# Performance work log

Measured on AMD Instinct MI355X. Metric: run time of the kernel, lower is better.

The kernel has to match this reference:

```python
import jax, jax.numpy as jnp
import numpy as np

B, S, E, H = 4, 2048, 512, 8
D = E // H  # head dim
CDIM = 3


def setup_inputs() -> dict:
    key = jax.random.key(0)
    ks = jax.random.split(key, 16)
    inp = {
        'q': jax.random.normal(ks[0], (B, S, E), jnp.float32),
        'k': jax.random.normal(ks[1], (B, S, E), jnp.float32),
        'v': jax.random.normal(ks[2], (B, S, E), jnp.float32),
        'coords_q': jax.random.normal(ks[3], (B, S, CDIM), jnp.float32),
        'coords_k': jax.random.normal(ks[4], (B, S, CDIM), jnp.float32),
        'attn_mask': jax.random.randint(ks[5], (B, S, S), 0, 2).astype(bool),
        'alibi_mask': jax.random.randint(ks[6], (B, S, S), 0, 2).astype(bool),
        # per-head projection params, stacked over heads: [H, E, D]
        'Wq': jax.random.normal(ks[7], (H, E, D), jnp.float32) / np.sqrt(E),
        'bq': jnp.zeros((H, D), jnp.float32),
        'Wk': jax.random.normal(ks[8], (H, E, D), jnp.float32) / np.sqrt(E),
        'bk': jnp.zeros((H, D), jnp.float32),
        'Wv': jax.random.normal(ks[9], (H, E, D), jnp.float32) / np.sqrt(E),
        'bv': jnp.zeros((H, D), jnp.float32),
        # per-head ALiBi params; running_mean is a buffer (eval mode -> constant ones)
        'bias_scale': jax.random.uniform(ks[10], (H,), jnp.float32),
        'running_mean': jnp.ones((H,), jnp.float32),
        # output projection
        'fc_w': jax.random.normal(ks[11], (E, E), jnp.float32) / np.sqrt(E),
        'fc_b': jnp.zeros((E,), jnp.float32),
    }
    return inp


def reference(q, k, v, coords_q, coords_k, attn_mask, alibi_mask,
              Wq, bq, Wk, bk, Wv, bv, bias_scale, running_mean, fc_w, fc_b):
    # per-head projections, vectorized over heads: [B,H,S,D]
    qh = jnp.einsum('bse,hed->bhsd', q, Wq) + bq[None, :, None, :]
    kh = jnp.einsum('bse,hed->bhsd', k, Wk) + bk[None, :, None, :]
    vh = jnp.einsum('bse,hed->bhsd', v, Wv) + bv[None, :, None, :]

    # scaled dot-product logits: [B,H,Sq,Sk]
    logits = jnp.einsum('bhqd,bhkd->bhqk', qh, kh) * (D ** -0.5)
    weights = jax.nn.softmax(logits, axis=-1)

    # pairwise euclidean distances between coords: [B,Sq,Sk]
    diff = coords_q[:, :, None, :] - coords_k[:, None, :, :]
    dist = jnp.sqrt(jnp.sum(diff * diff, axis=-1))

    # per-head distance bias (eval: divide by running_mean buffer, scale by bias_scale)
    scale = (bias_scale / running_mean)[None, :, None, None]  # [1,H,1,1]
    scaled_dist = dist[:, None, :, :] * scale                  # [B,H,Sq,Sk]
    masked_dist = jnp.where(~alibi_mask[:, None, :, :], scaled_dist, 0.0)

    # post-softmax bias subtraction and masking (non-standard attention)
    masked = jnp.where(~attn_mask[:, None, :, :], weights - masked_dist, 0.0)

    att = jnp.einsum('bhqk,bhkd->bhqd', masked, vh)            # [B,H,S,D]
    att = att.transpose(0, 2, 1, 3).reshape(B, S, E)           # [B,S,E]
    return att @ fc_w.T + fc_b
```

## Files before the change

kernel.cpp:

```cpp
#include <hip/hip_runtime.h>

typedef unsigned short ushort;
typedef unsigned char uchar;
typedef unsigned long long u64;
typedef __attribute__((ext_vector_type(8))) short short8;
typedef __attribute__((ext_vector_type(4))) float f32x4;
typedef __attribute__((ext_vector_type(4))) unsigned int uint4v;

#define B_ 4
#define S_ 2048
#define E_ 512
#define H_ 8
#define D_ 64
#define LDT 40
#define LDF 68

__device__ inline ushort f2bf(float f) {
  union { float f; unsigned int u; } v; v.f = f;
  unsigned int u = v.u;
  unsigned int r = u + 0x7FFFu + ((u >> 16) & 1u);
  return (ushort)(r >> 16);
}

__device__ inline unsigned int cvt_pk_bf16(float a, float b) {
  unsigned int r;
  asm("v_cvt_pk_bf16_f32 %0, %1, %2" : "=v"(r) : "v"(a), "v"(b));
  return r;
}

__device__ inline float exp2_fast(float x) {
#if defined(__has_builtin)
#if __has_builtin(__builtin_amdgcn_exp2f)
  return __builtin_amdgcn_exp2f(x);
#else
  return __expf(x * 0.69314718056f);
#endif
#else
  return __expf(x * 0.69314718056f);
#endif
}

__device__ inline short8 mask_keep(short8 p, short8 a2) {
  union U { short8 s; uint4v u; } P, A;
  P.s = p; A.s = a2;
#pragma unroll
  for (int i = 0; i < 4; ++i) {
    unsigned int t = A.u[i] & 0x80008000u;
    unsigned int dm = (t >> 15) * 0xFFFFu;
    P.u[i] &= ~dm;
  }
  return P.s;
}

__device__ inline float dpp_sum16(float v) {
  union { float f; int i; } s, t;
  s.f = v;
  t.i = __builtin_amdgcn_update_dpp(0, s.i, 0x128, 0xf, 0xf, false); s.f += t.f;
  t.i = __builtin_amdgcn_update_dpp(0, s.i, 0x124, 0xf, 0xf, false); s.f += t.f;
  t.i = __builtin_amdgcn_update_dpp(0, s.i, 0x122, 0xf, 0xf, false); s.f += t.f;
  t.i = __builtin_amdgcn_update_dpp(0, s.i, 0x121, 0xf, 0xf, false); s.f += t.f;
  return s.f;
}

__global__ void detect_kernel(const uchar* __restrict__ am, int* flag) {
  __shared__ int s;
  if (threadIdx.x == 0) s = 0;
  __syncthreads();
  int x = 0;
  for (int p = threadIdx.x; p < 4096; p += 256)
    if (p & 3) x += am[p];
  atomicAdd(&s, x);
  __syncthreads();
  if (threadIdx.x == 0) *flag = (s == 0) ? 1 : 0;
}

__global__ __launch_bounds__(256) void convert_w_kernel(
    const float* __restrict__ Wq, const float* __restrict__ Wk, const float* __restrict__ Wv,
    ushort* __restrict__ wt) {
  const int p = blockIdx.y;
  const float* W = (p == 0) ? Wq : (p == 1) ? Wk : Wv;
  const int n = blockIdx.x;
  const int h = n >> 6, d = n & 63;
  ushort* o = wt + ((size_t)p * E_ + n) * E_;
  for (int e = threadIdx.x; e < E_; e += 256)
    o[e] = f2bf(W[((size_t)h * E_ + e) * D_ + d]);
}

__global__ __launch_bounds__(256) void convert_fcw_kernel(
    const float* __restrict__ fcw, ushort* __restrict__ fcwbf) {
  size_t base = ((size_t)blockIdx.x * 256 + threadIdx.x) * 8;
  float4 a = *(const float4*)&fcw[base];
  float4 b = *(const float4*)&fcw[base + 4];
  short8 o;
  o[0] = (short)f2bf(a.x); o[1] = (short)f2bf(a.y); o[2] = (short)f2bf(a.z); o[3] = (short)f2bf(a.w);
  o[4] = (short)f2bf(b.x); o[5] = (short)f2bf(b.y); o[6] = (short)f2bf(b.z); o[7] = (short)f2bf(b.w);
  *(short8*)&fcwbf[base] = o;
}

__global__ __launch_bounds__(256) void proj_gemm_kernel(
    const float* __restrict__ qx, const float* __restrict__ kx, const float* __restrict__ vx,
    const ushort* __restrict__ wt,
    const float* __restrict__ bq, const float* __restrict__ bk, const float* __restrict__ bv,
    ushort* __restrict__ qkv) {
  const int phys = blockIdx.x;
  const int logical = (phys & 7) * 96 + (phys >> 3);
  const int p = logical >> 8;
  const int rem = logical & 255;
  const int m0 = (rem >> 2) * 128, n0 = (rem & 3) * 128;

  const float* A   = (p == 0) ? qx : (p == 1) ? kx : vx;
  const ushort* Bt = wt + (size_t)p * (E_ * E_);
  const float* bias = (p == 0) ? bq : (p == 1) ? bk : bv;
  const float osc = (p == 0) ? 0.125f * 1.44269504f : 1.0f;
  ushort* out = qkv + (size_t)p * (B_ * H_ * S_ * D_);

  const int tid = threadIdx.x;
  const int w = tid >> 6, lane = tid & 63;
  const int g = lane >> 4, c = lane & 15;
  const int wr = w >> 1, wc = w & 1;

  __shared__ ushort As[128][LDT], Bs[128][LDT];

  f32x4 acc[4][4];
#pragma unroll
  for (int i = 0; i < 4; ++i)
#pragma unroll
    for (int j = 0; j < 4; ++j) acc[i][j] = (f32x4){0, 0, 0, 0};

  const int srow = tid >> 2, sc8 = (tid & 3) * 8;
  float4 pa0[2], pa1[2];
  short8 pb[2];
#pragma unroll
  for (int it = 0; it < 2; ++it) {
    const float* ap = &A[(size_t)(m0 + srow + 64 * it) * E_ + sc8];
    pa0[it] = *(const float4*)ap;
    pa1[it] = *(const float4*)(ap + 4);
    pb[it] = *(const short8*)&Bt[(size_t)(n0 + srow + 64 * it) * E_ + sc8];
  }

  for (int kk = 0; kk < E_; kk += 32) {
    __syncthreads();
#pragma unroll
    for (int it = 0; it < 2; ++it) {
      unsigned int r0 = cvt_pk_bf16(pa0[it].x, pa0[it].y), r1 = cvt_pk_bf16(pa0[it].z, pa0[it].w);
      unsigned int r2 = cvt_pk_bf16(pa1[it].x, pa1[it].y), r3 = cvt_pk_bf16(pa1[it].z, pa1[it].w);
      short8 av;
      av[0] = (short)(ushort)r0; av[1] = (short)(ushort)(r0 >> 16);
      av[2] = (short)(ushort)r1; av[3] = (short)(ushort)(r1 >> 16);
      av[4] = (short)(ushort)r2; av[5] = (short)(ushort)(r2 >> 16);
      av[6] = (short)(ushort)r3; av[7] = (short)(ushort)(r3 >> 16);
      *(short8*)&As[srow + 64 * it][sc8] = av;
      *(short8*)&Bs[srow + 64 * it][sc8] = pb[it];
    }
    __syncthreads();
    if (kk + 32 < E_) {
#pragma unroll
      for (int it = 0; it < 2; ++it) {
        const float* ap = &A[(size_t)(m0 + srow + 64 * it) * E_ + kk + 32 + sc8];
        pa0[it] = *(const float4*)ap;
        pa1[it] = *(const float4*)(ap + 4);
        pb[it] = *(const short8*)&Bt[(size_t)(n0 + srow + 64 * it) * E_ + kk + 32 + sc8];
      }
    }
    short8 af[4], bfr[4];
#pragma unroll
    for (int i = 0; i < 4; ++i) af[i] = *(const short8*)&As[wr * 64 + i * 16 + c][8 * g];
#pragma unroll
    for (int j = 0; j < 4; ++j) bfr[j] = *(const short8*)&Bs[wc * 64 + j * 16 + c][8 * g];
#pragma unroll
    for (int i = 0; i < 4; ++i)
#pragma unroll
      for (int j = 0; j < 4; ++j)
        acc[i][j] = __builtin_amdgcn_mfma_f32_16x16x32_bf16(af[i], bfr[j], acc[i][j], 0, 0, 0);
  }

#pragma unroll
  for (int i = 0; i < 4; ++i)
#pragma unroll
    for (int jj = 0; jj < 4; ++jj) {
      int grow = m0 + wr * 64 + i * 16 + 4 * g + jj;
      int b = grow >> 11, s = grow & 2047;
#pragma unroll
      for (int j = 0; j < 4; ++j) {
        int col = n0 + wc * 64 + j * 16 + c;
        int h = col >> 6, d = col & 63;
        out[(((size_t)(b * H_ + h)) * S_ + s) * D_ + d] = f2bf((acc[i][j][jj] + bias[col]) * osc);
      }
    }
}

__global__ __launch_bounds__(256) void transpose_v_kernel(
    const ushort* __restrict__ vh, ushort* __restrict__ vtg) {
  const int bh = blockIdx.y, s0 = blockIdx.x * 64;
  __shared__ ushort tile[64][70];
  const int tid = threadIdx.x;
#pragma unroll
  for (int it = 0; it < 2; ++it) {
    int chunk = tid + 256 * it;
    int r = chunk >> 3, c8 = chunk & 7;
    *(short8*)&tile[r][c8 * 8] = *(const short8*)&vh[((size_t)bh * S_ + s0 + r) * D_ + c8 * 8];
  }
  __syncthreads();
#pragma unroll
  for (int it = 0; it < 2; ++it) {
    int chunk = tid + 256 * it;
    int d = chunk >> 3, s8 = chunk & 7;
    short8 o;
#pragma unroll
    for (int j = 0; j < 8; ++j) o[j] = (short)tile[s8 * 8 + j][d];
    *(short8*)&vtg[((size_t)bh * D_ + d) * S_ + s0 + s8 * 8] = o;
  }
}

__global__ __launch_bounds__(256) void m2dist_kernel(
    const float* __restrict__ cq, const float* __restrict__ ck,
    const void* __restrict__ am_raw, const void* __restrict__ alm_raw,
    const int* __restrict__ flag,
    ushort* __restrict__ m2d) {
  const bool isInt = (*flag != 0);
  const int b = blockIdx.y, qi = blockIdx.x;
  const int k0 = threadIdx.x * 8;
  const size_t rowbase = ((size_t)b * S_ + qi) * S_;
  const float qx = cq[((size_t)b * S_ + qi) * 3 + 0];
  const float qy = cq[((size_t)b * S_ + qi) * 3 + 1];
  const float qz = cq[((size_t)b * S_ + qi) * 3 + 2];
  int a[8], al[8];
  if (isInt) {
    int4 A0 = *(const int4*)&((const int*)am_raw)[rowbase + k0];
    int4 A1 = *(const int4*)&((const int*)am_raw)[rowbase + k0 + 4];
    int4 L0 = *(const int4*)&((const int*)alm_raw)[rowbase + k0];
    int4 L1 = *(const int4*)&((const int*)alm_raw)[rowbase + k0 + 4];
    a[0]=A0.x; a[1]=A0.y; a[2]=A0.z; a[3]=A0.w; a[4]=A1.x; a[5]=A1.y; a[6]=A1.z; a[7]=A1.w;
    al[0]=L0.x; al[1]=L0.y; al[2]=L0.z; al[3]=L0.w; al[4]=L1.x; al[5]=L1.y; al[6]=L1.z; al[7]=L1.w;
  } else {
    u64 ab = *(const u64*)&((const uchar*)am_raw)[rowbase + k0];
    u64 lb = *(const u64*)&((const uchar*)alm_raw)[rowbase + k0];
#pragma unroll
    for (int j = 0; j < 8; ++j) { a[j] = (int)((ab >> (8 * j)) & 0xFF); al[j] = (int)((lb >> (8 * j)) & 0xFF); }
  }
  float c24[24];
  {
    const float* ckp = ck + ((size_t)b * S_ + k0) * 3;
#pragma unroll
    for (int t = 0; t < 6; ++t) {
      float4 cv = *(const float4*)(ckp + 4 * t);
      c24[4 * t] = cv.x; c24[4 * t + 1] = cv.y; c24[4 * t + 2] = cv.z; c24[4 * t + 3] = cv.w;
    }
  }
  float dist[8];
#pragma unroll
  for (int j = 0; j < 8; ++j) {
    const float dx = qx - c24[3 * j], dy = qy - c24[3 * j + 1], dz = qz - c24[3 * j + 2];
    dist[j] = sqrtf(dx * dx + dy * dy + dz * dz);
  }
  short8 md;
#pragma unroll
  for (int jp = 0; jp < 4; ++jp) {
    unsigned int r = cvt_pk_bf16(dist[2 * jp], dist[2 * jp + 1]);
    ushort v0 = (!a[2 * jp]     && !al[2 * jp])     ? (ushort)r         : (ushort)0;
    ushort v1 = (!a[2 * jp + 1] && !al[2 * jp + 1]) ? (ushort)(r >> 16) : (ushort)0;
    if (a[2 * jp])     v0 |= 0x8000u;
    if (a[2 * jp + 1]) v1 |= 0x8000u;
    md[2 * jp] = (short)v0; md[2 * jp + 1] = (short)v1;
  }
  *(short8*)&m2d[rowbase + k0] = md;
}

__global__ __launch_bounds__(256) void flash_kernel(
    const ushort* __restrict__ qh, const ushort* __restrict__ kh, const ushort* __restrict__ vtg,
    const ushort* __restrict__ m2d,
    const float* __restrict__ bscale, const float* __restrict__ rmean,
    ushort* __restrict__ attb) {
  const int flat = blockIdx.x;
  const int h = flat >> 6;
  const int grp = flat & 63;
  const int b = grp >> 4;
  const int qb = (grp & 15) * 128;
  const int bh = b * 8 + h;
  const int tid = threadIdx.x;
  const int w = tid >> 6, lane = tid & 63;
  const int g = lane >> 4, c = lane & 15;

  __shared__ ushort Kt[2][64][LDF];
  __shared__ ushort Vt[2][64][LDF];
  __shared__ ushort Pl[4][32][LDF];

  const size_t bhS = (size_t)bh * S_;
  const int qr0 = qb + 16 * w + c;
  const int qr1 = qr0 + 64;
  const short8 aq0 = *(const short8*)(qh + (bhS + qr0) * D_ + 8 * g);
  const short8 aq1 = *(const short8*)(qh + (bhS + qr0) * D_ + 8 * g + 32);
  const short8 aq2 = *(const short8*)(qh + (bhS + qr1) * D_ + 8 * g);
  const short8 aq3 = *(const short8*)(qh + (bhS + qr1) * D_ + 8 * g + 32);

  const int skr = tid >> 3, sc8 = (tid & 7) * 8;
  const ushort* pk0 = kh + (bhS + skr) * D_ + sc8;
  const ushort* pk1 = pk0 + 32 * D_;
  const ushort* pv0 = vtg + ((size_t)bh * D_ + skr) * S_ + sc8;
  const ushort* pv1 = pv0 + 32 * S_;
  const ushort* pm0 = m2d + ((size_t)b * S_ + qr0) * S_ + 8 * g;
  const ushort* pm1 = pm0 + 32;
  const ushort* pm2 = m2d + ((size_t)b * S_ + qr1) * S_ + 8 * g;
  const ushort* pm3 = pm2 + 32;

  f32x4 acc1g0[4], acc2g0[4], acc1g1[4], acc2g1[4];
#pragma unroll
  for (int t = 0; t < 4; ++t) {
    acc1g0[t] = (f32x4){0,0,0,0}; acc2g0[t] = (f32x4){0,0,0,0};
    acc1g1[t] = (f32x4){0,0,0,0}; acc2g1[t] = (f32x4){0,0,0,0};
  }
  float l0[4] = {0, 0, 0, 0}, l1[4] = {0, 0, 0, 0};

  *(short8*)&Kt[0][skr][sc8]      = *(const short8*)pk0;  pk0 += 64 * D_;
  *(short8*)&Kt[0][skr + 32][sc8] = *(const short8*)pk1;  pk1 += 64 * D_;
  *(short8*)&Vt[0][skr][sc8]      = *(const short8*)pv0;  pv0 += 64;
  *(short8*)&Vt[0][skr + 32][sc8] = *(const short8*)pv1;  pv1 += 64;
  short8 a2n0 = *(const short8*)pm0; pm0 += 64;
  short8 a2n1 = *(const short8*)pm1; pm1 += 64;
  short8 a2n2 = *(const short8*)pm2; pm2 += 64;
  short8 a2n3 = *(const short8*)pm3; pm3 += 64;
  short8 skn0 = *(const short8*)pk0;  pk0 += 64 * D_;
  short8 skn1 = *(const short8*)pk1;  pk1 += 64 * D_;
  short8 svn0 = *(const short8*)pv0;  pv0 += 64;
  short8 svn1 = *(const short8*)pv1;  pv1 += 64;
  __syncthreads();

  for (int kb = 0; kb < S_; kb += 64) {
    const int cur = (kb >> 6) & 1;
    short8 a2c0 = a2n0, a2c1 = a2n1, a2c2 = a2n2, a2c3 = a2n3;
    a2n0 = *(const short8*)pm0; pm0 += 64;
    a2n1 = *(const short8*)pm1; pm1 += 64;
    a2n2 = *(const short8*)pm2; pm2 += 64;
    a2n3 = *(const short8*)pm3; pm3 += 64;

    f32x4 sf0[4], sf1[4];
    __builtin_amdgcn_s_setprio(1);
#pragma unroll
    for (int t = 0; t < 4; ++t) {
      short8 b0 = *(const short8*)&Kt[cur][16 * t + c][8 * g];
      short8 b1 = *(const short8*)&Kt[cur][16 * t + c][8 * g + 32];
      f32x4 z0 = (f32x4){0, 0, 0, 0}, z1 = (f32x4){0, 0, 0, 0};
      z0 = __builtin_amdgcn_mfma_f32_16x16x32_bf16(aq0, b0, z0, 0, 0, 0);
      z0 = __builtin_amdgcn_mfma_f32_16x16x32_bf16(aq1, b1, z0, 0, 0, 0);
      z1 = __builtin_amdgcn_mfma_f32_16x16x32_bf16(aq2, b0, z1, 0, 0, 0);
      z1 = __builtin_amdgcn_mfma_f32_16x16x32_bf16(aq3, b1, z1, 0, 0, 0);
      sf0[t] = z0; sf1[t] = z1;
    }
    __builtin_amdgcn_s_setprio(0);

#pragma unroll
    for (int t = 0; t < 4; ++t)
#pragma unroll
      for (int jp = 0; jp < 2; ++jp) {
        float p0 = exp2_fast(sf0[t][2 * jp]);
        float p1 = exp2_fast(sf0[t][2 * jp + 1]);
        l0[2 * jp] += p0; l0[2 * jp + 1] += p1;
        unsigned int r = cvt_pk_bf16(p0, p1);
        Pl[w][4 * g + 2 * jp][16 * t + c]     = (ushort)r;
        Pl[w][4 * g + 2 * jp + 1][16 * t + c] = (ushort)(r >> 16);
        float p2 = exp2_fast(sf1[t][2 * jp]);
        float p3 = exp2_fast(sf1[t][2 * jp + 1]);
        l1[2 * jp] += p2; l1[2 * jp + 1] += p3;
        unsigned int r2 = cvt_pk_bf16(p2, p3);
        Pl[w][16 + 4 * g + 2 * jp][16 * t + c]     = (ushort)r2;
        Pl[w][16 + 4 * g + 2 * jp + 1][16 * t + c] = (ushort)(r2 >> 16);
      }

    asm volatile("s_waitcnt lgkmcnt(0)" ::: "memory");
    __builtin_amdgcn_sched_barrier(0);

    short8 pa0 = *(const short8*)&Pl[w][c][8 * g];
    short8 pa1 = *(const short8*)&Pl[w][c][8 * g + 32];
    short8 pa2 = *(const short8*)&Pl[w][16 + c][8 * g];
    short8 pa3 = *(const short8*)&Pl[w][16 + c][8 * g + 32];
    pa0 = mask_keep(pa0, a2c0);
    pa1 = mask_keep(pa1, a2c1);
    pa2 = mask_keep(pa2, a2c2);
    pa3 = mask_keep(pa3, a2c3);
    __builtin_amdgcn_s_setprio(1);
#pragma unroll
    for (int t2 = 0; t2 < 4; ++t2) {
      short8 v0 = *(const short8*)&Vt[cur][16 * t2 + c][8 * g];
      short8 v1 = *(const short8*)&Vt[cur][16 * t2 + c][8 * g + 32];
      acc1g0[t2] = __builtin_amdgcn_mfma_f32_16x16x32_bf16(pa0, v0, acc1g0[t2], 0, 0, 0);
      acc1g0[t2] = __builtin_amdgcn_mfma_f32_16x16x32_bf16(pa1, v1, acc1g0[t2], 0, 0, 0);
      acc2g0[t2] = __builtin_amdgcn_mfma_f32_16x16x32_bf16(a2c0, v0, acc2g0[t2], 0, 0, 0);
      acc2g0[t2] = __builtin_amdgcn_mfma_f32_16x16x32_bf16(a2c1, v1, acc2g0[t2], 0, 0, 0);
      acc1g1[t2] = __builtin_amdgcn_mfma_f32_16x16x32_bf16(pa2, v0, acc1g1[t2], 0, 0, 0);
      acc1g1[t2] = __builtin_amdgcn_mfma_f32_16x16x32_bf16(pa3, v1, acc1g1[t2], 0, 0, 0);
      acc2g1[t2] = __builtin_amdgcn_mfma_f32_16x16x32_bf16(a2c2, v0, acc2g1[t2], 0, 0, 0);
      acc2g1[t2] = __builtin_amdgcn_mfma_f32_16x16x32_bf16(a2c3, v1, acc2g1[t2], 0, 0, 0);
    }
    __builtin_amdgcn_s_setprio(0);

    if (kb + 64 < S_) {
      *(short8*)&Kt[cur ^ 1][skr][sc8]      = skn0;
      *(short8*)&Kt[cur ^ 1][skr + 32][sc8] = skn1;
      *(short8*)&Vt[cur ^ 1][skr][sc8]      = svn0;
      *(short8*)&Vt[cur ^ 1][skr + 32][sc8] = svn1;
      skn0 = *(const short8*)pk0;  pk0 += 64 * D_;
      skn1 = *(const short8*)pk1;  pk1 += 64 * D_;
      svn0 = *(const short8*)pv0;  pv0 += 64;
      svn1 = *(const short8*)pv1;  pv1 += 64;
    }
    __syncthreads();
  }

  float linv0[4], linv1[4];
#pragma unroll
  for (int j = 0; j < 4; ++j) {
    linv0[j] = 1.0f / dpp_sum16(l0[j]);
    linv1[j] = 1.0f / dpp_sum16(l1[j]);
  }
  const float scale = bscale[h] / rmean[h];
#pragma unroll
  for (int t2 = 0; t2 < 4; ++t2)
#pragma unroll
    for (int j = 0; j < 4; ++j) {
      int qrA = qb + 16 * w + 4 * g + j;
      int d = 16 * t2 + c;
      attb[(((size_t)b * S_ + qrA) * H_ + h) * D_ + d] =
          f2bf(acc1g0[t2][j] * linv0[j] - scale * acc2g0[t2][j]);
      attb[(((size_t)b * S_ + qrA + 64) * H_ + h) * D_ + d] =
          f2bf(acc1g1[t2][j] * linv1[j] - scale * acc2g1[t2][j]);
    }
}

__global__ __launch_bounds__(256) void final_gemm_kernel(
    const ushort* __restrict__ attb, const ushort* __restrict__ fcwbf,
    const float* __restrict__ fcb, float* __restrict__ out) {
  const int phys = blockIdx.x;
  const int logical = (phys & 7) * 32 + (phys >> 3);
  const int m0 = (logical >> 2) * 128, n0 = (logical & 3) * 128;
  const int tid = threadIdx.x;
  const int w = tid >> 6, lane = tid & 63;
  const int g = lane >> 4, c = lane & 15;
  const int wr = w >> 1, wc = w & 1;

  __shared__ ushort As[128][LDT], Bs[128][LDT];

  f32x4 acc[4][4];
#pragma unroll
  for (int i = 0; i < 4; ++i)
#pragma unroll
    for (int j = 0; j < 4; ++j) acc[i][j] = (f32x4){0, 0, 0, 0};

  const int srow = tid >> 2, sc8 = (tid & 3) * 8;
  short8 pa[2], pb[2];
#pragma unroll
  for (int it = 0; it < 2; ++it) {
    pa[it] = *(const short8*)&attb[(size_t)(m0 + srow + 64 * it) * E_ + sc8];
    pb[it] = *(const short8*)&fcwbf[(size_t)(n0 + srow + 64 * it) * E_ + sc8];
  }

  for (int kk = 0; kk < E_; kk += 32) {
    __syncthreads();
#pragma unroll
    for (int it = 0; it < 2; ++it) {
      *(short8*)&As[srow + 64 * it][sc8] = pa[it];
      *(short8*)&Bs[srow + 64 * it][sc8] = pb[it];
    }
    __syncthreads();
    if (kk + 32 < E_) {
#pragma unroll
      for (int it = 0; it < 2; ++it) {
        pa[it] = *(const short8*)&attb[(size_t)(m0 + srow + 64 * it) * E_ + kk + 32 + sc8];
        pb[it] = *(const short8*)&fcwbf[(size_t)(n0 + srow + 64 * it) * E_ + kk + 32 + sc8];
      }
    }
    short8 af[4], bfr[4];
#pragma unroll
    for (int i = 0; i < 4; ++i) af[i] = *(const short8*)&As[wr * 64 + i * 16 + c][8 * g];
#pragma unroll
    for (int j = 0; j < 4; ++j) bfr[j] = *(const short8*)&Bs[wc * 64 + j * 16 + c][8 * g];
#pragma unroll
    for (int i = 0; i < 4; ++i)
#pragma unroll
      for (int j = 0; j < 4; ++j)
        acc[i][j] = __builtin_amdgcn_mfma_f32_16x16x32_bf16(af[i], bfr[j], acc[i][j], 0, 0, 0);
  }

#pragma unroll
  for (int i = 0; i < 4; ++i)
#pragma unroll
    for (int jj = 0; jj < 4; ++jj) {
      int grow = m0 + wr * 64 + i * 16 + 4 * g + jj;
#pragma unroll
      for (int j = 0; j < 4; ++j) {
        int col = n0 + wc * 64 + j * 16 + c;
        out[(size_t)grow * E_ + col] = acc[i][j][jj] + fcb[col];
      }
    }
}

extern "C" void kernel_launch(void* const* d_in, const int* in_sizes, int n_in,
                              void* d_out, int out_size, void* d_ws, size_t ws_size,
                              hipStream_t stream) {
  const float* q   = (const float*)d_in[0];
  const float* k   = (const float*)d_in[1];
  const float* v   = (const float*)d_in[2];
  const float* cq  = (const float*)d_in[3];
  const float* ck  = (const float*)d_in[4];
  const void*  am  = d_in[5];
  const void*  alm = d_in[6];
  const float* Wq  = (const float*)d_in[7];
  const float* bq  = (const float*)d_in[8];
  const float* Wk  = (const float*)d_in[9];
  const float* bk  = (const float*)d_in[10];
  const float* Wv  = (const float*)d_in[11];
  const float* bv  = (const float*)d_in[12];
  const float* bsc = (const float*)d_in[13];
  const float* rm  = (const float*)d_in[14];
  const float* fcw = (const float*)d_in[15];
  const float* fcb = (const float*)d_in[16];
  float* out = (float*)d_out;

  char* ws = (char*)d_ws;
  ushort* attb = (ushort*)(ws);
  ushort* vtg  = (ushort*)(ws + 16ull * 1024 * 1024);
  ushort* qkv  = (ushort*)(ws + 24ull * 1024 * 1024);
  ushort* m2d  = (ushort*)(ws + 48ull * 1024 * 1024);
  ushort* wt   = (ushort*)(ws + 80ull * 1024 * 1024);
  ushort* fcwbf= (ushort*)(ws + 80ull * 1024 * 1024 + 1536 * 1024);
  int*    flag = (int*)   (ws + 82ull * 1024 * 1024);

  ushort* qh = qkv;
  ushort* kh = qkv + (size_t)(B_ * H_ * S_ * D_);
  ushort* vh = qkv + 2 * (size_t)(B_ * H_ * S_ * D_);

  detect_kernel<<<1, 256, 0, stream>>>((const uchar*)am, flag);
  convert_w_kernel<<<dim3(512, 3), 256, 0, stream>>>(Wq, Wk, Wv, wt);
  convert_fcw_kernel<<<128, 256, 0, stream>>>(fcw, fcwbf);
  proj_gemm_kernel<<<768, 256, 0, stream>>>(q, k, v, wt, bq, bk, bv, qkv);
  transpose_v_kernel<<<dim3(S_ / 64, B_ * H_), 256, 0, stream>>>(vh, vtg);
  m2dist_kernel<<<dim3(S_, B_), 256, 0, stream>>>(cq, ck, am, alm, flag, m2d);
  flash_kernel<<<512, 256, 0, stream>>>(qh, kh, vtg, m2d, bsc, rm, attb);
  final_gemm_kernel<<<256, 256, 0, stream>>>(attb, fcwbf, fcb, out);
}
```

Baseline: 176.6 us.

## Split key range across two wave groups in flash kernel with LDS reduction

Doubles the flash attention block to 512 threads: two groups of four waves each handle alternating 64-key tiles for the same query rows, then combine their accumulators and row sums through shared memory. The probability tile buffer is halved and the two query sub-tiles are processed one after another. K/V staging moves from LDS double buffering to register prefetch with two barriers per iteration. This aims to raise wave-level parallelism and latency hiding, at the cost of extra syncs, a final reduction, and more serialized exp/MFMA phases.

```diff
diff --git a/kernel.cpp b/kernel.cpp
--- a/kernel.cpp
+++ b/kernel.cpp
@@ -266,7 +266,7 @@
   *(short8*)&m2d[rowbase + k0] = md;
 }
 
-__global__ __launch_bounds__(256) void flash_kernel(
+__global__ __launch_bounds__(512) void flash_kernel(
     const ushort* __restrict__ qh, const ushort* __restrict__ kh, const ushort* __restrict__ vtg,
     const ushort* __restrict__ m2d,
     const float* __restrict__ bscale, const float* __restrict__ rmean,
@@ -280,13 +280,14 @@
   const int tid = threadIdx.x;
   const int w = tid >> 6, lane = tid & 63;
   const int g = lane >> 4, c = lane & 15;
-
-  __shared__ ushort Kt[2][64][LDF];
-  __shared__ ushort Vt[2][64][LDF];
-  __shared__ ushort Pl[4][32][LDF];
+  const int wq = w & 3, wh = w >> 2;
+
+  __shared__ __align__(16) ushort Kt[2][64][LDF];
+  __shared__ __align__(16) ushort Vt[2][64][LDF];
+  __shared__ __align__(16) ushort Pl[8][16][LDF];
 
   const size_t bhS = (size_t)bh * S_;
-  const int qr0 = qb + 16 * w + c;
+  const int qr0 = qb + 16 * wq + c;
   const int qr1 = qr0 + 64;
   const short8 aq0 = *(const short8*)(qh + (bhS + qr0) * D_ + 8 * g);
   const short8 aq1 = *(const short8*)(qh + (bhS + qr0) * D_ + 8 * g + 32);
@@ -295,12 +296,12 @@
 
   const int skr = tid >> 3, sc8 = (tid & 7) * 8;
   const ushort* pk0 = kh + (bhS + skr) * D_ + sc8;
-  const ushort* pk1 = pk0 + 32 * D_;
+  const ushort* pk1 = pk0 + 64 * D_;
   const ushort* pv0 = vtg + ((size_t)bh * D_ + skr) * S_ + sc8;
-  const ushort* pv1 = pv0 + 32 * S_;
-  const ushort* pm0 = m2d + ((size_t)b * S_ + qr0) * S_ + 8 * g;
+  const ushort* pv1 = pv0 + 64;
+  const ushort* pm0 = m2d + ((size_t)b * S_ + qr0) * S_ + wh * 64 + 8 * g;
   const ushort* pm1 = pm0 + 32;
-  const ushort* pm2 = m2d + ((size_t)b * S_ + qr1) * S_ + 8 * g;
+  const ushort* pm2 = m2d + ((size_t)b * S_ + qr1) * S_ + wh * 64 + 8 * g;
   const ushort* pm3 = pm2 + 32;
 
   f32x4 acc1g0[4], acc2g0[4], acc1g1[4], acc2g1[4];
@@ -311,34 +312,39 @@
   }
   float l0[4] = {0, 0, 0, 0}, l1[4] = {0, 0, 0, 0};
 
-  *(short8*)&Kt[0][skr][sc8]      = *(const short8*)pk0;  pk0 += 64 * D_;
-  *(short8*)&Kt[0][skr + 32][sc8] = *(const short8*)pk1;  pk1 += 64 * D_;
-  *(short8*)&Vt[0][skr][sc8]      = *(const short8*)pv0;  pv0 += 64;
-  *(short8*)&Vt[0][skr + 32][sc8] = *(const short8*)pv1;  pv1 += 64;
-  short8 a2n0 = *(const short8*)pm0; pm0 += 64;
-  short8 a2n1 = *(const short8*)pm1; pm1 += 64;
-  short8 a2n2 = *(const short8*)pm2; pm2 += 64;
-  short8 a2n3 = *(const short8*)pm3; pm3 += 64;
-  short8 skn0 = *(const short8*)pk0;  pk0 += 64 * D_;
-  short8 skn1 = *(const short8*)pk1;  pk1 += 64 * D_;
-  short8 svn0 = *(const short8*)pv0;  pv0 += 64;
-  short8 svn1 = *(const short8*)pv1;  pv1 += 64;
-  __syncthreads();
-
-  for (int kb = 0; kb < S_; kb += 64) {
-    const int cur = (kb >> 6) & 1;
+  short8 sk0 = *(const short8*)pk0;  pk0 += 128 * D_;
+  short8 sk1 = *(const short8*)pk1;  pk1 += 128 * D_;
+  short8 sv0 = *(const short8*)pv0;  pv0 += 128;
+  short8 sv1 = *(const short8*)pv1;  pv1 += 128;
+  short8 a2n0 = *(const short8*)pm0; pm0 += 128;
+  short8 a2n1 = *(const short8*)pm1; pm1 += 128;
+  short8 a2n2 = *(const short8*)pm2; pm2 += 128;
+  short8 a2n3 = *(const short8*)pm3; pm3 += 128;
+
+  for (int i = 0; i < 16; ++i) {
+    __syncthreads();
+    *(short8*)&Kt[0][skr][sc8] = sk0;
+    *(short8*)&Kt[1][skr][sc8] = sk1;
+    *(short8*)&Vt[0][skr][sc8] = sv0;
+    *(short8*)&Vt[1][skr][sc8] = sv1;
+    __syncthreads();
+
     short8 a2c0 = a2n0, a2c1 = a2n1, a2c2 = a2n2, a2c3 = a2n3;
-    a2n0 = *(const short8*)pm0; pm0 += 64;
-    a2n1 = *(const short8*)pm1; pm1 += 64;
-    a2n2 = *(const short8*)pm2; pm2 += 64;
-    a2n3 = *(const short8*)pm3; pm3 += 64;
+    sk0 = *(const short8*)pk0;  pk0 += 128 * D_;
+    sk1 = *(const short8*)pk1;  pk1 += 128 * D_;
+    sv0 = *(const short8*)pv0;  pv0 += 128;
+    sv1 = *(const short8*)pv1;  pv1 += 128;
+    a2n0 = *(const short8*)pm0; pm0 += 128;
+    a2n1 = *(const short8*)pm1; pm1 += 128;
+    a2n2 = *(const short8*)pm2; pm2 += 128;
+    a2n3 = *(const short8*)pm3; pm3 += 128;
 
     f32x4 sf0[4], sf1[4];
     __builtin_amdgcn_s_setprio(1);
 #pragma unroll
     for (int t = 0; t < 4; ++t) {
-      short8 b0 = *(const short8*)&Kt[cur][16 * t + c][8 * g];
-      short8 b1 = *(const short8*)&Kt[cur][16 * t + c][8 * g + 32];
+      short8 b0 = *(const short8*)&Kt[wh][16 * t + c][8 * g];
+      short8 b1 = *(const short8*)&Kt[wh][16 * t + c][8 * g + 32];
       f32x4 z0 = (f32x4){0, 0, 0, 0}, z1 = (f32x4){0, 0, 0, 0};
       z0 = __builtin_amdgcn_mfma_f32_16x16x32_bf16(aq0, b0, z0, 0, 0, 0);
       z0 = __builtin_amdgcn_mfma_f32_16x16x32_bf16(aq1, b1, z0, 0, 0, 0);
@@ -358,30 +364,39 @@
         unsigned int r = cvt_pk_bf16(p0, p1);
         Pl[w][4 * g + 2 * jp][16 * t + c]     = (ushort)r;
         Pl[w][4 * g + 2 * jp + 1][16 * t + c] = (ushort)(r >> 16);
-        float p2 = exp2_fast(sf1[t][2 * jp]);
-        float p3 = exp2_fast(sf1[t][2 * jp + 1]);
-        l1[2 * jp] += p2; l1[2 * jp + 1] += p3;
-        unsigned int r2 = cvt_pk_bf16(p2, p3);
-        Pl[w][16 + 4 * g + 2 * jp][16 * t + c]     = (ushort)r2;
-        Pl[w][16 + 4 * g + 2 * jp + 1][16 * t + c] = (ushort)(r2 >> 16);
-      }
-
+      }
     asm volatile("s_waitcnt lgkmcnt(0)" ::: "memory");
     __builtin_amdgcn_sched_barrier(0);
-
     short8 pa0 = *(const short8*)&Pl[w][c][8 * g];
     short8 pa1 = *(const short8*)&Pl[w][c][8 * g + 32];
-    short8 pa2 = *(const short8*)&Pl[w][16 + c][8 * g];
-    short8 pa3 = *(const short8*)&Pl[w][16 + c][8 * g + 32];
     pa0 = mask_keep(pa0, a2c0);
     pa1 = mask_keep(pa1, a2c1);
+    asm volatile("s_waitcnt lgkmcnt(0)" ::: "memory");
+    __builtin_amdgcn_sched_barrier(0);
+
+#pragma unroll
+    for (int t = 0; t < 4; ++t)
+#pragma unroll
+      for (int jp = 0; jp < 2; ++jp) {
+        float p0 = exp2_fast(sf1[t][2 * jp]);
+        float p1 = exp2_fast(sf1[t][2 * jp + 1]);
+        l1[2 * jp] += p0; l1[2 * jp + 1] += p1;
+        unsigned int r = cvt_pk_bf16(p0, p1);
+        Pl[w][4 * g + 2 * jp][16 * t + c]     = (ushort)r;
+        Pl[w][4 * g + 2 * jp + 1][16 * t + c] = (ushort)(r >> 16);
+      }
+    asm volatile("s_waitcnt lgkmcnt(0)" ::: "memory");
+    __builtin_amdgcn_sched_barrier(0);
+    short8 pa2 = *(const short8*)&Pl[w][c][8 * g];
+    short8 pa3 = *(const short8*)&Pl[w][c][8 * g + 32];
     pa2 = mask_keep(pa2, a2c2);
     pa3 = mask_keep(pa3, a2c3);
+
     __builtin_amdgcn_s_setprio(1);
 #pragma unroll
     for (int t2 = 0; t2 < 4; ++t2) {
-      short8 v0 = *(const short8*)&Vt[cur][16 * t2 + c][8 * g];
-      short8 v1 = *(const short8*)&Vt[cur][16 * t2 + c][8 * g + 32];
+      short8 v0 = *(const short8*)&Vt[wh][16 * t2 + c][8 * g];
+      short8 v1 = *(const short8*)&Vt[wh][16 * t2 + c][8 * g + 32];
       acc1g0[t2] = __builtin_amdgcn_mfma_f32_16x16x32_bf16(pa0, v0, acc1g0[t2], 0, 0, 0);
       acc1g0[t2] = __builtin_amdgcn_mfma_f32_16x16x32_bf16(pa1, v1, acc1g0[t2], 0, 0, 0);
       acc2g0[t2] = __builtin_amdgcn_mfma_f32_16x16x32_bf16(a2c0, v0, acc2g0[t2], 0, 0, 0);
@@ -392,38 +407,67 @@
       acc2g1[t2] = __builtin_amdgcn_mfma_f32_16x16x32_bf16(a2c3, v1, acc2g1[t2], 0, 0, 0);
     }
     __builtin_amdgcn_s_setprio(0);
-
-    if (kb + 64 < S_) {
-      *(short8*)&Kt[cur ^ 1][skr][sc8]      = skn0;
-      *(short8*)&Kt[cur ^ 1][skr + 32][sc8] = skn1;
-      *(short8*)&Vt[cur ^ 1][skr][sc8]      = svn0;
-      *(short8*)&Vt[cur ^ 1][skr + 32][sc8] = svn1;
-      skn0 = *(const short8*)pk0;  pk0 += 64 * D_;
-      skn1 = *(const short8*)pk1;  pk1 += 64 * D_;
-      svn0 = *(const short8*)pv0;  pv0 += 64;
-      svn1 = *(const short8*)pv1;  pv1 += 64;
-    }
-    __syncthreads();
-  }
-
-  float linv0[4], linv1[4];
-#pragma unroll
-  for (int j = 0; j < 4; ++j) {
-    linv0[j] = 1.0f / dpp_sum16(l0[j]);
-    linv1[j] = 1.0f / dpp_sum16(l1[j]);
-  }
-  const float scale = bscale[h] / rmean[h];
-#pragma unroll
-  for (int t2 = 0; t2 < 4; ++t2)
+  }
+
+  float* cA = (float*)&Kt[0][0][0];
+  float* cB = (float*)&Vt[0][0][0];
+  float* cC = (float*)&Pl[0][0][0];
+  const int cidx = (wq * 64 + lane) * 16;
+  __syncthreads();
+  if (wh == 1) {
+#pragma unroll
+    for (int t = 0; t < 4; ++t) {
+      *(f32x4*)&cA[cidx + 4 * t] = acc1g0[t];
+      *(f32x4*)&cB[cidx + 4 * t] = acc1g1[t];
+      *(f32x4*)&cC[cidx + 4 * t] = acc2g0[t];
+    }
+  }
+  __syncthreads();
+  if (wh == 0) {
+#pragma unroll
+    for (int t = 0; t < 4; ++t) {
+      acc1g0[t] += *(const f32x4*)&cA[cidx + 4 * t];
+      acc1g1[t] += *(const f32x4*)&cB[cidx + 4 * t];
+      acc2g0[t] += *(const f32x4*)&cC[cidx + 4 * t];
+    }
+  }
+  __syncthreads();
+  if (wh == 1) {
+#pragma unroll
+    for (int t = 0; t < 4; ++t) *(f32x4*)&cA[cidx + 4 * t] = acc2g1[t];
+    f32x4 lv0 = (f32x4){l0[0], l0[1], l0[2], l0[3]};
+    f32x4 lv1 = (f32x4){l1[0], l1[1], l1[2], l1[3]};
+    *(f32x4*)&cB[(wq * 64 + lane) * 8]     = lv0;
+    *(f32x4*)&cB[(wq * 64 + lane) * 8 + 4] = lv1;
+  }
+  __syncthreads();
+  if (wh == 0) {
+#pragma unroll
+    for (int t = 0; t < 4; ++t) acc2g1[t] += *(const f32x4*)&cA[cidx + 4 * t];
+    f32x4 lv0 = *(const f32x4*)&cB[(wq * 64 + lane) * 8];
+    f32x4 lv1 = *(const f32x4*)&cB[(wq * 64 + lane) * 8 + 4];
+#pragma unroll
+    for (int j = 0; j < 4; ++j) { l0[j] += lv0[j]; l1[j] += lv1[j]; }
+
+    float linv0[4], linv1[4];
 #pragma unroll
     for (int j = 0; j < 4; ++j) {
-      int qrA = qb + 16 * w + 4 * g + j;
-      int d = 16 * t2 + c;
-      attb[(((size_t)b * S_ + qrA) * H_ + h) * D_ + d] =
-          f2bf(acc1g0[t2][j] * linv0[j] - scale * acc2g0[t2][j]);
-      attb[(((size_t)b * S_ + qrA + 64) * H_ + h) * D_ + d] =
-          f2bf(acc1g1[t2][j] * linv1[j] - scale * acc2g1[t2][j]);
-    }
+      linv0[j] = 1.0f / dpp_sum16(l0[j]);
+      linv1[j] = 1.0f / dpp_sum16(l1[j]);
+    }
+    const float scale = bscale[h] / rmean[h];
+#pragma unroll
+    for (int t2 = 0; t2 < 4; ++t2)
+#pragma unroll
+      for (int j = 0; j < 4; ++j) {
+        int qrA = qb + 16 * wq + 4 * g + j;
+        int d = 16 * t2 + c;
+        attb[(((size_t)b * S_ + qrA) * H_ + h) * D_ + d] =
+            f2bf(acc1g0[t2][j] * linv0[j] - scale * acc2g0[t2][j]);
+        attb[(((size_t)b * S_ + qrA + 64) * H_ + h) * D_ + d] =
+            f2bf(acc1g1[t2][j] * linv1[j] - scale * acc2g1[t2][j]);
+      }
+  }
 }
 
 __global__ __launch_bounds__(256) void final_gemm_kernel(
@@ -534,6 +578,6 @@
   proj_gemm_kernel<<<768, 256, 0, stream>>>(q, k, v, wt, bq, bk, bv, qkv);
   transpose_v_kernel<<<dim3(S_ / 64, B_ * H_), 256, 0, stream>>>(vh, vtg);
   m2dist_kernel<<<dim3(S_, B_), 256, 0, stream>>>(cq, ck, am, alm, flag, m2d);
-  flash_kernel<<<512, 256, 0, stream>>>(qh, kh, vtg, m2d, bsc, rm, attb);
+  flash_kernel<<<512, 512, 0, stream>>>(qh, kh, vtg, m2d, bsc, rm, attb);
   final_gemm_kernel<<<256, 256, 0, stream>>>(attb, fcwbf, fcb, out);
 }
```

New measurement: 189.1 us. 1.07x slower.
